# Optimization experiments

Hardware: AMD Instinct MI355X
Metric: run time of the kernel (lower is better)

## Reference

```python
import jax, jax.numpy as jnp
from jax import lax
import numpy as np

NUM_CLASSES = 80
STRIDES = (8, 16, 32)
CONF_THRE = 0.01
NMS_THRE = 0.65
TOPK = 500  # fixed pre-NMS candidate cap (jit-compatible stand-in for dynamic conf filter)


def setup_inputs() -> dict:
    key = jax.random.key(0)
    k8, k16, k32 = jax.random.split(key, 3)
    B, C = 8, 5 + NUM_CLASSES
    return {
        "out8": jax.random.normal(k8, (B, C, 160, 160), dtype=jnp.float32),
        "out16": jax.random.normal(k16, (B, C, 80, 80), dtype=jnp.float32),
        "out32": jax.random.normal(k32, (B, C, 40, 40), dtype=jnp.float32),
    }


def _decode_level(x, stride):
    # x: [B, C, H, W] -> decoded [B, H*W, C]
    B, C, H, W = x.shape
    x = x.reshape(B, C, H * W).transpose(0, 2, 1)  # [B, HW, C]
    yv, xv = jnp.meshgrid(jnp.arange(H), jnp.arange(W), indexing="ij")
    grid = jnp.stack([xv, yv], axis=-1).reshape(1, H * W, 2).astype(x.dtype)
    s = jnp.asarray(stride, x.dtype)
    xy = (x[..., 0:2] + grid) * s
    wh = jnp.exp(x[..., 2:4]) * s
    obj = jax.nn.sigmoid(x[..., 4:5])
    cls = jax.nn.sigmoid(x[..., 5:])
    return jnp.concatenate([xy, wh, obj, cls], axis=-1)


def _iou_one_vs_all(box, boxes):
    # box: [4] xyxy, boxes: [K,4] xyxy
    x1 = jnp.maximum(box[0], boxes[:, 0])
    y1 = jnp.maximum(box[1], boxes[:, 1])
    x2 = jnp.minimum(box[2], boxes[:, 2])
    y2 = jnp.minimum(box[3], boxes[:, 3])
    inter = jnp.maximum(x2 - x1, 0.0) * jnp.maximum(y2 - y1, 0.0)
    a1 = jnp.maximum(box[2] - box[0], 0.0) * jnp.maximum(box[3] - box[1], 0.0)
    a2 = jnp.maximum(boxes[:, 2] - boxes[:, 0], 0.0) * jnp.maximum(boxes[:, 3] - boxes[:, 1], 0.0)
    return inter / (a1 + a2 - inter + 1e-9)


def _nms_keep(boxes, valid, iou_thr):
    # boxes are pre-sorted by descending score; returns bool keep mask [K]
    K = boxes.shape[0]
    idx = jnp.arange(K)

    def body(i, state):
        keep, suppressed = state
        cur_ok = jnp.logical_not(suppressed[i])
        keep = keep.at[i].set(cur_ok)
        iou = _iou_one_vs_all(boxes[i], boxes)
        suppressed = suppressed | ((iou > iou_thr) & cur_ok & (idx > i))
        return keep, suppressed

    keep, _ = lax.fori_loop(0, K, body, (jnp.zeros(K, bool), jnp.logical_not(valid)))
    return keep


def _post_process_image(pred):
    # pred: [N, 5+num_classes] decoded, boxes already xyxy
    cls_scores = pred[:, 5:5 + NUM_CLASSES]
    class_conf = jnp.max(cls_scores, axis=1)
    class_pred = jnp.argmax(cls_scores, axis=1)
    obj = pred[:, 4]
    total = obj * class_conf  # NMS score, same as torchvision call
    masked = jnp.where(total >= CONF_THRE, total, -1.0)
    top_sc, top_i = lax.top_k(masked, TOPK)  # sorted descending
    boxes = pred[top_i, :4]
    obj_k = obj[top_i]
    cc_k = class_conf[top_i]
    lab_k = class_pred[top_i]
    valid = top_sc >= CONF_THRE
    # class-aware (batched) NMS via per-class coordinate offset, as torchvision does
    max_c = jnp.max(jnp.where(valid[:, None], boxes, 0.0)) + 1.0
    boxes_off = boxes + (lab_k.astype(boxes.dtype) * max_c)[:, None]
    keep = _nms_keep(boxes_off, valid, NMS_THRE)
    det = jnp.concatenate(
        [boxes, obj_k[:, None], cc_k[:, None], lab_k.astype(boxes.dtype)[:, None]], axis=1
    )  # [K, 7] = (x1,y1,x2,y2,obj,class_conf,class_id)
    return det * keep[:, None].astype(det.dtype)


def reference(out8, out16, out32):
    levels = [(out8, 8), (out16, 16), (out32, 32)]
    pred = jnp.concatenate([_decode_level(x, s) for x, s in levels], axis=1)  # [B, N, C]
    # cxcywh -> xyxy corners
    cx, cy, w, h = pred[..., 0], pred[..., 1], pred[..., 2], pred[..., 3]
    corners = jnp.stack([cx - w / 2, cy - h / 2, cx + w / 2, cy + h / 2], axis=-1)
    pred = jnp.concatenate([corners, pred[..., 4:]], axis=-1)
    return jax.vmap(_post_process_image)(pred)  # [B, TOPK, 7], zero-padded
```

## Files before the change

### kernel.cpp

```cpp
#include <hip/hip_runtime.h>

#define NPI    33600
#define KTOP   500
#define CAP    1024
#define KEY001 0xBC23D70Au
#define NGRP   1024
#define NIMG   8
#define GPW    525

__device__ __forceinline__ float sigmoidf_(float x) {
  return 1.0f / (1.0f + expf(-x));
}
__device__ __forceinline__ unsigned fkey(float f) {
  unsigned u = __float_as_uint(f);
  return (u & 0x80000000u) ? ~u : (u | 0x80000000u);
}

__global__ __launch_bounds__(128) void k_decode(
    const float* __restrict__ p8, const float* __restrict__ p16,
    const float* __restrict__ p32,
    unsigned* __restrict__ keys, float* __restrict__ dets,
    unsigned* __restrict__ hist2)
{
  const int b  = blockIdx.y;
  const int tx = blockIdx.x;
  const float* lvl; int HW, W, S, j0, abase;
  if (tx < 50)      { lvl = p8;  HW = 25600; W = 160; S = 8;  j0 = tx * 512;        abase = 0; }
  else if (tx < 63) { lvl = p16; HW = 6400;  W = 80;  S = 16; j0 = (tx - 50) * 512; abase = 25600; }
  else              { lvl = p32; HW = 1600;  W = 40;  S = 32; j0 = (tx - 63) * 512; abase = 32000; }
  __shared__ unsigned lh[NGRP];
  for (int i = threadIdx.x; i < NGRP; i += 128) lh[i] = 0;
  __syncthreads();

  const int e = j0 + 4 * threadIdx.x;
  const bool act = (e < HW);
  if (act) {
    const float* base = lvl + (size_t)b * 85 * HW + e;
    float4 t0 = *(const float4*)(base);
    float4 t1 = *(const float4*)(base + (size_t)1 * HW);
    float4 t2 = *(const float4*)(base + (size_t)2 * HW);
    float4 t3 = *(const float4*)(base + (size_t)3 * HW);
    float4 t4 = *(const float4*)(base + (size_t)4 * HW);
    float cc[4] = {-1.0f, -1.0f, -1.0f, -1.0f};
    int   lab[4] = {0, 0, 0, 0};
    for (int c0 = 5; c0 < 85; c0 += 16) {
      float4 r[16];
      #pragma unroll
      for (int u = 0; u < 16; ++u)
        r[u] = *(const float4*)(base + (size_t)(c0 + u) * HW);
      #pragma unroll
      for (int u = 0; u < 16; ++u) {
        float s;
        s = sigmoidf_(r[u].x); if (s > cc[0]) { cc[0] = s; lab[0] = c0 + u - 5; }
        s = sigmoidf_(r[u].y); if (s > cc[1]) { cc[1] = s; lab[1] = c0 + u - 5; }
        s = sigmoidf_(r[u].z); if (s > cc[2]) { cc[2] = s; lab[2] = c0 + u - 5; }
        s = sigmoidf_(r[u].w); if (s > cc[3]) { cc[3] = s; lab[3] = c0 + u - 5; }
      }
    }
    float e0[4] = {t0.x, t0.y, t0.z, t0.w};
    float e1[4] = {t1.x, t1.y, t1.z, t1.w};
    float e2[4] = {t2.x, t2.y, t2.z, t2.w};
    float e3[4] = {t3.x, t3.y, t3.z, t3.w};
    float e4[4] = {t4.x, t4.y, t4.z, t4.w};
    unsigned k4[4];
    float dv[7][4];
    #pragma unroll
    for (int q = 0; q < 4; ++q) {
      float obj = sigmoidf_(e4[q]);
      float tot = obj * cc[q];
      k4[q] = fkey(tot >= 0.01f ? tot : -1.0f);
      int jj = e + q;
      int gy = jj / W, gx = jj - gy * W;
      float fs = (float)S;
      float cx = (e0[q] + (float)gx) * fs;
      float cy = (e1[q] + (float)gy) * fs;
      float w  = expf(e2[q]) * fs;
      float h  = expf(e3[q]) * fs;
      dv[0][q] = cx - 0.5f * w; dv[1][q] = cy - 0.5f * h;
      dv[2][q] = cx + 0.5f * w; dv[3][q] = cy + 0.5f * h;
      dv[4][q] = obj; dv[5][q] = cc[q]; dv[6][q] = (float)lab[q];
    }
    const int a = abase + e;
    *(uint4*)(keys + (size_t)b * NPI + a) = make_uint4(k4[0], k4[1], k4[2], k4[3]);
    const size_t P  = (size_t)NIMG * NPI;
    const size_t pa = (size_t)b * NPI + a;
    #pragma unroll
    for (int c = 0; c < 7; ++c)
      *(float4*)(dets + (size_t)c * P + pa) =
          make_float4(dv[c][0], dv[c][1], dv[c][2], dv[c][3]);
    #pragma unroll
    for (int q = 0; q < 4; ++q) atomicAdd(&lh[k4[q] >> 22], 1u);
  }
  __syncthreads();
  unsigned* gb = hist2 + (size_t)b * NGRP;
  for (int i = threadIdx.x; i < NGRP; i += 128) {
    unsigned v = lh[i];
    if (v) atomicAdd(&gb[i], v);
  }
}

__global__ __launch_bounds__(1024) void k_select(
    const unsigned* __restrict__ hist2, const unsigned* __restrict__ keys,
    const float* __restrict__ dets,
    float* __restrict__ topdet, float* __restrict__ soa,
    unsigned* __restrict__ invalg)
{
  const int b    = blockIdx.x;
  const int tid  = threadIdx.x;
  const int lane = tid & 63;
  const int wave = tid >> 6;

  __shared__ unsigned lh[NGRP];
  __shared__ unsigned sh_sub[4096];
  __shared__ unsigned sh_c64[64];
  __shared__ unsigned sh_G, sh_T;
  __shared__ __align__(16) unsigned long long sh_cand[CAP];
  __shared__ float sh_det[KTOP][7];
  __shared__ unsigned sh_inval[16];
  __shared__ unsigned sh_wcA[16], sh_wcB[16];
  __shared__ float sh_red[16];
  __shared__ float sh_maxc;

  lh[tid] = hist2[(size_t)b * NGRP + tid];
  for (int i = tid; i < 4096; i += 1024) sh_sub[i] = 0;
  __syncthreads();
  if (tid < 64) {
    unsigned s = 0;
    #pragma unroll
    for (int k = 0; k < 16; ++k) s += lh[tid * 16 + k];
    sh_c64[tid] = s;
  }
  __syncthreads();
  if (tid == 0) {
    unsigned cum = 0; int C = 0;
    for (int g = 63; g >= 0; --g) {
      unsigned v = sh_c64[g];
      if (cum + v >= KTOP) { C = g; break; }
      cum += v;
    }
    int G = C * 16; unsigned chi = cum;
    for (int g = C * 16 + 15; g >= C * 16; --g) {
      unsigned v = lh[g];
      if (chi + v >= KTOP) { G = g; break; }
      chi += v;
    }
    sh_G = (unsigned)G;
    sh_c64[0] = chi;
  }
  __syncthreads();
  const unsigned G = sh_G;
  const unsigned* kb = keys + (size_t)b * NPI;

  for (int g = tid; g < NPI / 4; g += 1024) {
    uint4 kv = ((const uint4*)kb)[g];
    unsigned kk[4] = {kv.x, kv.y, kv.z, kv.w};
    #pragma unroll
    for (int q = 0; q < 4; ++q)
      if ((kk[q] >> 22) == G) atomicAdd(&sh_sub[(kk[q] >> 10) & 4095u], 1u);
  }
  __syncthreads();
  unsigned chi10 = sh_c64[0];
  __syncthreads();
  if (tid < 64) {
    unsigned s = 0;
    for (int k = 0; k < 64; ++k) s += sh_sub[tid * 64 + k];
    sh_c64[tid] = s;
  }
  __syncthreads();
  if (tid == 0) {
    unsigned c = chi10; int C2 = 0;
    for (int g = 63; g >= 0; --g) {
      unsigned v = sh_c64[g];
      if (c + v >= KTOP) { C2 = g; break; }
      c += v;
    }
    int T12 = C2 * 64;
    for (int t2 = C2 * 64 + 63; t2 >= C2 * 64; --t2) {
      unsigned v = sh_sub[t2];
      if (c + v >= KTOP) { T12 = t2; break; }
      c += v;
    }
    sh_T = (G << 12) | (unsigned)T12;
  }
  __syncthreads();
  const unsigned T = sh_T;

  unsigned runA = 0, runB = 0;
  for (int it = 0; it < 9; ++it) {
    int gl = it * 64 + lane;
    bool act = (gl < GPW);
    int g = wave * GPW + gl;
    uint4 kv = act ? ((const uint4*)kb)[g] : make_uint4(0, 0, 0, 0);
    unsigned kk[4] = {kv.x, kv.y, kv.z, kv.w};
    #pragma unroll
    for (int q = 0; q < 4; ++q) {
      unsigned bin = kk[q] >> 10;
      runA += (unsigned)__popcll(__ballot(act && (bin > T)));
      runB += (unsigned)__popcll(__ballot(act && (bin == T)));
    }
  }
  if (lane == 0) { sh_wcA[wave] = runA; sh_wcB[wave] = runB; }
  __syncthreads();
  unsigned pA = 0, pB = 0, nA = 0, nBtot = 0;
  #pragma unroll
  for (int w2 = 0; w2 < 16; ++w2) {
    unsigned va = sh_wcA[w2], vb = sh_wcB[w2];
    if (w2 < wave) { pA += va; pB += vb; }
    nA += va; nBtot += vb;
  }
  const unsigned Bcap = CAP - nA;
  const unsigned nBk  = (nBtot < Bcap) ? nBtot : Bcap;
  const int nTot = (int)(nA + nBk);

  for (int it = 0; it < 9; ++it) {
    int gl = it * 64 + lane;
    bool act = (gl < GPW);
    int g = wave * GPW + gl;
    uint4 kv = act ? ((const uint4*)kb)[g] : make_uint4(0, 0, 0, 0);
    unsigned kk[4] = {kv.x, kv.y, kv.z, kv.w};
    bool iA[4], iB[4];
    unsigned long long balA[4], balB[4];
    #pragma unroll
    for (int q = 0; q < 4; ++q) {
      unsigned bin = kk[q] >> 10;
      iA[q] = act && (bin > T);
      iB[q] = act && (bin == T);
      balA[q] = __ballot(iA[q]);
      balB[q] = __ballot(iB[q]);
    }
    unsigned long long lt = (1ULL << lane) - 1ULL;
    unsigned pAl = pA, pBl = pB;
    #pragma unroll
    for (int q = 0; q < 4; ++q) {
      pAl += (unsigned)__popcll(balA[q] & lt);
      pBl += (unsigned)__popcll(balB[q] & lt);
    }
    #pragma unroll
    for (int q = 0; q < 4; ++q) {
      int a0 = g * 4 + q;
      unsigned long long packed =
          ((unsigned long long)kk[q] << 32) |
          (unsigned long long)(0xFFFFFFFFu - (unsigned)a0);
      if (iA[q]) { sh_cand[pAl] = packed; ++pAl; }
      if (iB[q]) { if (pBl < Bcap) sh_cand[nA + pBl] = packed; ++pBl; }
      pA += (unsigned)__popcll(balA[q]);
      pB += (unsigned)__popcll(balB[q]);
    }
  }
  __syncthreads();
  for (int s = nTot + tid; s < CAP; s += 1024) sh_cand[s] = 0ULL;
  __syncthreads();

  for (unsigned kk2 = 2; kk2 <= CAP; kk2 <<= 1) {
    for (unsigned jj = kk2 >> 1; jj > 0; jj >>= 1) {
      unsigned i = (unsigned)tid, p = i ^ jj;
      if (p > i) {
        unsigned long long x = sh_cand[i], y = sh_cand[p];
        bool desc = ((i & kk2) == 0);
        if ((x < y) == desc) { sh_cand[i] = y; sh_cand[p] = x; }
      }
      __syncthreads();
    }
  }

  bool validk = false;
  float contrib = -INFINITY;
  float det[7] = {0, 0, 0, 0, 0, 0, 0};
  if (tid < KTOP) {
    unsigned long long v = sh_cand[tid];
    unsigned keyk = (unsigned)(v >> 32);
    int a = (int)(0xFFFFFFFFu - (unsigned)(v & 0xFFFFFFFFull));
    if (a < 0) a = 0;
    const size_t P  = (size_t)NIMG * NPI;
    const size_t pa = (size_t)b * NPI + (size_t)a;
    #pragma unroll
    for (int c = 0; c < 7; ++c) det[c] = dets[(size_t)c * P + pa];
    #pragma unroll
    for (int c = 0; c < 7; ++c) sh_det[tid][c] = det[c];
    validk = (keyk >= KEY001);
    float m4 = fmaxf(fmaxf(det[0], det[1]), fmaxf(det[2], det[3]));
    contrib = validk ? m4 : 0.0f;
  }
  float r = contrib;
  #pragma unroll
  for (int off = 32; off > 0; off >>= 1) r = fmaxf(r, __shfl_xor(r, off));
  if (lane == 0) sh_red[wave] = r;
  unsigned long long bv = __ballot((tid < KTOP) && !validk);
  if (wave < 8 && lane == 0) {
    sh_inval[wave * 2]     = (unsigned)(bv & 0xFFFFFFFFull);
    sh_inval[wave * 2 + 1] = (unsigned)(bv >> 32);
  }
  __syncthreads();
  if (tid == 0) {
    float m = -INFINITY;
    for (int w2 = 0; w2 < 16; ++w2) m = fmaxf(m, sh_red[w2]);
    sh_maxc = m + 1.0f;
  }
  __syncthreads();
  const float maxc = sh_maxc;
  if (tid < 512) {
    float x1, y1, x2, y2, ar;
    if (tid < KTOP) {
      float offb = det[6] * maxc;
      x1 = det[0] + offb; y1 = det[1] + offb;
      x2 = det[2] + offb; y2 = det[3] + offb;
      ar = fmaxf(x2 - x1, 0.0f) * fmaxf(y2 - y1, 0.0f);
    } else { x1 = y1 = x2 = y2 = ar = 0.0f; }
    soa[(0 * NIMG + b) * 512 + tid] = x1;
    soa[(1 * NIMG + b) * 512 + tid] = y1;
    soa[(2 * NIMG + b) * 512 + tid] = x2;
    soa[(3 * NIMG + b) * 512 + tid] = y2;
    soa[(4 * NIMG + b) * 512 + tid] = ar;
  }
  if (tid < 16) invalg[b * 16 + tid] = sh_inval[tid];
  for (int x = tid; x < KTOP * 7; x += 1024)
    topdet[(size_t)b * (KTOP * 7) + x] = ((const float*)sh_det)[x];
}

__global__ __launch_bounds__(256) void k_iou(
    const float* __restrict__ soa, unsigned* __restrict__ gmask)
{
  const int w = blockIdx.x, b = blockIdx.y;
  const int tid = threadIdx.x;
  __shared__ float sx1[512], sy1[512], sx2[512], sy2[512], sa[512];
  for (int x = tid; x < 512; x += 256) {
    sx1[x] = soa[(0 * NIMG + b) * 512 + x];
    sy1[x] = soa[(1 * NIMG + b) * 512 + x];
    sx2[x] = soa[(2 * NIMG + b) * 512 + x];
    sy2[x] = soa[(3 * NIMG + b) * 512 + x];
    sa[x]  = soa[(4 * NIMG + b) * 512 + x];
  }
  __syncthreads();
  const int jbase = w * 32;
  for (int i = tid; i < KTOP; i += 256) {
    unsigned bits = 0u;
    if (jbase + 31 > i) {
      float ix1 = sx1[i], iy1 = sy1[i], ix2 = sx2[i], iy2 = sy2[i];
      float a1 = sa[i];
      #pragma unroll 4
      for (int jj = 0; jj < 32; ++jj) {
        int j = jbase + jj;
        if (j < KTOP && j > i) {
          float jx1 = sx1[j], jy1 = sy1[j];
          float jx2 = sx2[j], jy2 = sy2[j];
          float a2  = sa[j];
          float iw = fminf(ix2, jx2) - fmaxf(ix1, jx1);
          float ih = fminf(iy2, jy2) - fmaxf(iy1, jy1);
          float inter = fmaxf(iw, 0.0f) * fmaxf(ih, 0.0f);
          if (inter > 0.65f * (a1 + a2 - inter + 1e-9f)) bits |= (1u << jj);
        }
      }
    }
    gmask[((size_t)b * 16 + w) * 512 + i] = bits;
  }
}

__global__ __launch_bounds__(256) void k_nms(
    const unsigned* __restrict__ gmask, const unsigned* __restrict__ invalg,
    const float* __restrict__ topdet, float* __restrict__ out)
{
  const int b = blockIdx.x;
  const int tid = threadIdx.x;
  const int lane = tid & 63;
  __shared__ unsigned sm[KTOP * 17];
  __shared__ unsigned sh_keep[16];
  for (int g = tid; g < KTOP * 16; g += 256) {
    int w = g / KTOP, i = g - w * KTOP;
    sm[i * 17 + w] = gmask[((size_t)b * 16 + w) * 512 + i];
  }
  __syncthreads();
  if (tid < 64) {
    unsigned sup   = (lane < 16) ? invalg[b * 16 + lane] : 0u;
    unsigned keepw = 0u;
    unsigned cur = (unsigned)__builtin_amdgcn_readlane((int)sup, 0);
    unsigned mA = (lane < 16) ? sm[0 * 17 + lane] : 0u;
    unsigned mB = (lane < 16) ? sm[1 * 17 + lane] : 0u;
    for (int i = 0; i < KTOP; i += 2) {
      bool ok = ((cur >> (i & 31)) & 1u) == 0u;
      if (ok) {
        sup |= mA;
        if (lane == (i >> 5)) keepw |= (1u << (i & 31));
      }
      cur = (unsigned)__builtin_amdgcn_readlane((int)sup, (i + 1) >> 5);
      mA = (lane < 16 && (i + 2) < KTOP) ? sm[(i + 2) * 17 + lane] : 0u;
      bool ok2 = ((cur >> ((i + 1) & 31)) & 1u) == 0u;
      if (ok2) {
        sup |= mB;
        if (lane == ((i + 1) >> 5)) keepw |= (1u << ((i + 1) & 31));
      }
      cur = (unsigned)__builtin_amdgcn_readlane((int)sup, (i + 2) >> 5);
      mB = (lane < 16 && (i + 3) < KTOP) ? sm[(i + 3) * 17 + lane] : 0u;
    }
    if (lane < 16) sh_keep[lane] = keepw;
  }
  __syncthreads();
  for (int x = tid; x < KTOP * 7; x += 256) {
    int k = x / 7;
    float keepf = ((sh_keep[k >> 5] >> (k & 31)) & 1u) ? 1.0f : 0.0f;
    out[(size_t)b * (KTOP * 7) + x] = topdet[(size_t)b * (KTOP * 7) + x] * keepf;
  }
}

extern "C" void kernel_launch(void* const* d_in, const int* in_sizes, int n_in,
                              void* d_out, int out_size, void* d_ws, size_t ws_size,
                              hipStream_t stream) {
  const float* p8  = (const float*)d_in[0];
  const float* p16 = (const float*)d_in[1];
  const float* p32 = (const float*)d_in[2];
  float* out = (float*)d_out;
  unsigned* hist2  = (unsigned*)d_ws;
  unsigned* keys   = hist2 + (size_t)NIMG * NGRP;
  float*    dets   = (float*)(keys + (size_t)NIMG * NPI);
  float*    topdet = dets + (size_t)7 * NIMG * NPI;
  float*    soa    = topdet + (size_t)NIMG * KTOP * 7;
  unsigned* invalg = (unsigned*)(soa + (size_t)5 * NIMG * 512);
  unsigned* gmask  = invalg + NIMG * 16;

  hipMemsetAsync(hist2, 0, (size_t)NIMG * NGRP * 4, stream);
  k_decode<<<dim3(67, NIMG), 128, 0, stream>>>(p8, p16, p32, keys, dets, hist2);
  k_select<<<dim3(NIMG), 1024, 0, stream>>>(hist2, keys, dets, topdet, soa, invalg);
  k_iou<<<dim3(16, NIMG), 256, 0, stream>>>(soa, gmask);
  k_nms<<<dim3(NIMG), 256, 0, stream>>>(gmask, invalg, topdet, out);
}
```

Before: 210.0 us.

## Score anchors with raw max-logit and decode only the selected top-K boxes

```diff
diff --git a/kernel.cpp b/kernel.cpp
--- a/kernel.cpp
+++ b/kernel.cpp
@@ -16,84 +16,45 @@
   return (u & 0x80000000u) ? ~u : (u | 0x80000000u);
 }
 
-__global__ __launch_bounds__(128) void k_decode(
+__global__ __launch_bounds__(256) void k_score(
     const float* __restrict__ p8, const float* __restrict__ p16,
     const float* __restrict__ p32,
-    unsigned* __restrict__ keys, float* __restrict__ dets,
-    unsigned* __restrict__ hist2)
+    unsigned* __restrict__ keys, unsigned* __restrict__ hist2)
 {
   const int b  = blockIdx.y;
   const int tx = blockIdx.x;
-  const float* lvl; int HW, W, S, j0, abase;
-  if (tx < 50)      { lvl = p8;  HW = 25600; W = 160; S = 8;  j0 = tx * 512;        abase = 0; }
-  else if (tx < 63) { lvl = p16; HW = 6400;  W = 80;  S = 16; j0 = (tx - 50) * 512; abase = 25600; }
-  else              { lvl = p32; HW = 1600;  W = 40;  S = 32; j0 = (tx - 63) * 512; abase = 32000; }
+  const float* lvl; int HW, j0, abase;
+  if (tx < 50)      { lvl = p8;  HW = 25600; j0 = tx * 512;        abase = 0; }
+  else if (tx < 63) { lvl = p16; HW = 6400;  j0 = (tx - 50) * 512; abase = 25600; }
+  else              { lvl = p32; HW = 1600;  j0 = (tx - 63) * 512; abase = 32000; }
   __shared__ unsigned lh[NGRP];
-  for (int i = threadIdx.x; i < NGRP; i += 128) lh[i] = 0;
-  __syncthreads();
-
-  const int e = j0 + 4 * threadIdx.x;
-  const bool act = (e < HW);
-  if (act) {
+  for (int i = threadIdx.x; i < NGRP; i += 256) lh[i] = 0;
+  __syncthreads();
+
+  const int e = j0 + 2 * threadIdx.x;
+  if (e < HW) {
     const float* base = lvl + (size_t)b * 85 * HW + e;
-    float4 t0 = *(const float4*)(base);
-    float4 t1 = *(const float4*)(base + (size_t)1 * HW);
-    float4 t2 = *(const float4*)(base + (size_t)2 * HW);
-    float4 t3 = *(const float4*)(base + (size_t)3 * HW);
-    float4 t4 = *(const float4*)(base + (size_t)4 * HW);
-    float cc[4] = {-1.0f, -1.0f, -1.0f, -1.0f};
-    int   lab[4] = {0, 0, 0, 0};
+    float2 o2 = *(const float2*)(base + (size_t)4 * HW);
+    float m0 = -INFINITY, m1 = -INFINITY;
     for (int c0 = 5; c0 < 85; c0 += 16) {
-      float4 r[16];
+      float2 r[16];
       #pragma unroll
       for (int u = 0; u < 16; ++u)
-        r[u] = *(const float4*)(base + (size_t)(c0 + u) * HW);
+        r[u] = *(const float2*)(base + (size_t)(c0 + u) * HW);
       #pragma unroll
-      for (int u = 0; u < 16; ++u) {
-        float s;
-        s = sigmoidf_(r[u].x); if (s > cc[0]) { cc[0] = s; lab[0] = c0 + u - 5; }
-        s = sigmoidf_(r[u].y); if (s > cc[1]) { cc[1] = s; lab[1] = c0 + u - 5; }
-        s = sigmoidf_(r[u].z); if (s > cc[2]) { cc[2] = s; lab[2] = c0 + u - 5; }
-        s = sigmoidf_(r[u].w); if (s > cc[3]) { cc[3] = s; lab[3] = c0 + u - 5; }
-      }
-    }
-    float e0[4] = {t0.x, t0.y, t0.z, t0.w};
-    float e1[4] = {t1.x, t1.y, t1.z, t1.w};
-    float e2[4] = {t2.x, t2.y, t2.z, t2.w};
-    float e3[4] = {t3.x, t3.y, t3.z, t3.w};
-    float e4[4] = {t4.x, t4.y, t4.z, t4.w};
-    unsigned k4[4];
-    float dv[7][4];
-    #pragma unroll
-    for (int q = 0; q < 4; ++q) {
-      float obj = sigmoidf_(e4[q]);
-      float tot = obj * cc[q];
-      k4[q] = fkey(tot >= 0.01f ? tot : -1.0f);
-      int jj = e + q;
-      int gy = jj / W, gx = jj - gy * W;
-      float fs = (float)S;
-      float cx = (e0[q] + (float)gx) * fs;
-      float cy = (e1[q] + (float)gy) * fs;
-      float w  = expf(e2[q]) * fs;
-      float h  = expf(e3[q]) * fs;
-      dv[0][q] = cx - 0.5f * w; dv[1][q] = cy - 0.5f * h;
-      dv[2][q] = cx + 0.5f * w; dv[3][q] = cy + 0.5f * h;
-      dv[4][q] = obj; dv[5][q] = cc[q]; dv[6][q] = (float)lab[q];
-    }
-    const int a = abase + e;
-    *(uint4*)(keys + (size_t)b * NPI + a) = make_uint4(k4[0], k4[1], k4[2], k4[3]);
-    const size_t P  = (size_t)NIMG * NPI;
-    const size_t pa = (size_t)b * NPI + a;
-    #pragma unroll
-    for (int c = 0; c < 7; ++c)
-      *(float4*)(dets + (size_t)c * P + pa) =
-          make_float4(dv[c][0], dv[c][1], dv[c][2], dv[c][3]);
-    #pragma unroll
-    for (int q = 0; q < 4; ++q) atomicAdd(&lh[k4[q] >> 22], 1u);
+      for (int u = 0; u < 16; ++u) { m0 = fmaxf(m0, r[u].x); m1 = fmaxf(m1, r[u].y); }
+    }
+    float s0 = sigmoidf_(o2.x) * sigmoidf_(m0);
+    float s1 = sigmoidf_(o2.y) * sigmoidf_(m1);
+    unsigned k0 = fkey(s0 >= 0.01f ? s0 : -1.0f);
+    unsigned k1 = fkey(s1 >= 0.01f ? s1 : -1.0f);
+    *(uint2*)(keys + (size_t)b * NPI + abase + e) = make_uint2(k0, k1);
+    atomicAdd(&lh[k0 >> 22], 1u);
+    atomicAdd(&lh[k1 >> 22], 1u);
   }
   __syncthreads();
   unsigned* gb = hist2 + (size_t)b * NGRP;
-  for (int i = threadIdx.x; i < NGRP; i += 128) {
+  for (int i = threadIdx.x; i < NGRP; i += 256) {
     unsigned v = lh[i];
     if (v) atomicAdd(&gb[i], v);
   }
@@ -101,9 +62,7 @@
 
 __global__ __launch_bounds__(1024) void k_select(
     const unsigned* __restrict__ hist2, const unsigned* __restrict__ keys,
-    const float* __restrict__ dets,
-    float* __restrict__ topdet, float* __restrict__ soa,
-    unsigned* __restrict__ invalg)
+    unsigned* __restrict__ selanch, unsigned* __restrict__ invalg)
 {
   const int b    = blockIdx.x;
   const int tid  = threadIdx.x;
@@ -115,11 +74,8 @@
   __shared__ unsigned sh_c64[64];
   __shared__ unsigned sh_G, sh_T;
   __shared__ __align__(16) unsigned long long sh_cand[CAP];
-  __shared__ float sh_det[KTOP][7];
   __shared__ unsigned sh_inval[16];
   __shared__ unsigned sh_wcA[16], sh_wcB[16];
-  __shared__ float sh_red[16];
-  __shared__ float sh_maxc;
 
   lh[tid] = hist2[(size_t)b * NGRP + tid];
   for (int i = tid; i < 4096; i += 1024) sh_sub[i] = 0;
@@ -263,72 +219,121 @@
     }
   }
 
-  bool validk = false;
-  float contrib = -INFINITY;
-  float det[7] = {0, 0, 0, 0, 0, 0, 0};
   if (tid < KTOP) {
     unsigned long long v = sh_cand[tid];
     unsigned keyk = (unsigned)(v >> 32);
     int a = (int)(0xFFFFFFFFu - (unsigned)(v & 0xFFFFFFFFull));
     if (a < 0) a = 0;
-    const size_t P  = (size_t)NIMG * NPI;
-    const size_t pa = (size_t)b * NPI + (size_t)a;
-    #pragma unroll
-    for (int c = 0; c < 7; ++c) det[c] = dets[(size_t)c * P + pa];
-    #pragma unroll
-    for (int c = 0; c < 7; ++c) sh_det[tid][c] = det[c];
-    validk = (keyk >= KEY001);
-    float m4 = fmaxf(fmaxf(det[0], det[1]), fmaxf(det[2], det[3]));
-    contrib = validk ? m4 : 0.0f;
-  }
-  float r = contrib;
-  #pragma unroll
-  for (int off = 32; off > 0; off >>= 1) r = fmaxf(r, __shfl_xor(r, off));
-  if (lane == 0) sh_red[wave] = r;
-  unsigned long long bv = __ballot((tid < KTOP) && !validk);
-  if (wave < 8 && lane == 0) {
-    sh_inval[wave * 2]     = (unsigned)(bv & 0xFFFFFFFFull);
-    sh_inval[wave * 2 + 1] = (unsigned)(bv >> 32);
-  }
-  __syncthreads();
-  if (tid == 0) {
-    float m = -INFINITY;
-    for (int w2 = 0; w2 < 16; ++w2) m = fmaxf(m, sh_red[w2]);
-    sh_maxc = m + 1.0f;
-  }
-  __syncthreads();
-  const float maxc = sh_maxc;
-  if (tid < 512) {
-    float x1, y1, x2, y2, ar;
-    if (tid < KTOP) {
-      float offb = det[6] * maxc;
-      x1 = det[0] + offb; y1 = det[1] + offb;
-      x2 = det[2] + offb; y2 = det[3] + offb;
-      ar = fmaxf(x2 - x1, 0.0f) * fmaxf(y2 - y1, 0.0f);
-    } else { x1 = y1 = x2 = y2 = ar = 0.0f; }
-    soa[(0 * NIMG + b) * 512 + tid] = x1;
-    soa[(1 * NIMG + b) * 512 + tid] = y1;
-    soa[(2 * NIMG + b) * 512 + tid] = x2;
-    soa[(3 * NIMG + b) * 512 + tid] = y2;
-    soa[(4 * NIMG + b) * 512 + tid] = ar;
-  }
+    selanch[b * KTOP + tid] = (unsigned)a;
+    bool validk = (keyk >= KEY001);
+    unsigned long long bv = __ballot(!validk);
+    if (lane == 0) {
+      sh_inval[wave * 2]     = (unsigned)(bv & 0xFFFFFFFFull);
+      sh_inval[wave * 2 + 1] = (unsigned)(bv >> 32);
+    }
+  } else {
+    unsigned long long bv = __ballot(false);
+    (void)bv;
+  }
+  __syncthreads();
   if (tid < 16) invalg[b * 16 + tid] = sh_inval[tid];
-  for (int x = tid; x < KTOP * 7; x += 1024)
-    topdet[(size_t)b * (KTOP * 7) + x] = ((const float*)sh_det)[x];
+}
+
+__global__ __launch_bounds__(256) void k_gather(
+    const float* __restrict__ p8, const float* __restrict__ p16,
+    const float* __restrict__ p32,
+    const unsigned* __restrict__ selanch, float* __restrict__ seldet)
+{
+  const int b    = blockIdx.y;
+  const int part = blockIdx.x;
+  const int tid  = threadIdx.x;
+  const int p    = tid & 15;
+  const int grp  = tid >> 4;
+  const int lane = tid & 63;
+  const int g0   = lane & ~15;
+
+  for (int iter = 0; iter < 4; ++iter) {
+    int s = part * 64 + iter * 16 + grp;
+    if (s >= KTOP) continue;
+    int a = (int)selanch[b * KTOP + s];
+    const float* lvl; int j, W, HW, S;
+    if (a < 25600)      { lvl = p8;  j = a;         W = 160; HW = 25600; S = 8;  }
+    else if (a < 32000) { lvl = p16; j = a - 25600; W = 80;  HW = 6400;  S = 16; }
+    else                { lvl = p32; j = a - 32000; W = 40;  HW = 1600;  S = 32; }
+    const float* base = lvl + (size_t)b * 85 * HW + j;
+    float cc = -1.0f; int lab = 0;
+    #pragma unroll
+    for (int u = 0; u < 5; ++u) {
+      int c = p + 16 * u;
+      float sv = sigmoidf_(base[(size_t)(5 + c) * HW]);
+      if (sv > cc) { cc = sv; lab = c; }
+    }
+    float tload = (p < 5) ? base[(size_t)p * HW] : 0.0f;
+    #pragma unroll
+    for (int off = 1; off < 16; off <<= 1) {
+      float occ = __shfl_xor(cc, off);
+      int  olb = __shfl_xor(lab, off);
+      if (occ > cc || (occ == cc && olb < lab)) { cc = occ; lab = olb; }
+    }
+    float t0 = __shfl(tload, g0 + 0);
+    float t1 = __shfl(tload, g0 + 1);
+    float t2 = __shfl(tload, g0 + 2);
+    float t3 = __shfl(tload, g0 + 3);
+    float t4 = __shfl(tload, g0 + 4);
+    if (p == 0) {
+      int gy = j / W, gx = j - gy * W;
+      float fs = (float)S;
+      float cx = (t0 + (float)gx) * fs;
+      float cy = (t1 + (float)gy) * fs;
+      float w  = expf(t2) * fs;
+      float h  = expf(t3) * fs;
+      float obj = sigmoidf_(t4);
+      float* d = seldet + ((size_t)b * KTOP + s) * 7;
+      d[0] = cx - 0.5f * w; d[1] = cy - 0.5f * h;
+      d[2] = cx + 0.5f * w; d[3] = cy + 0.5f * h;
+      d[4] = obj; d[5] = cc; d[6] = (float)lab;
+    }
+  }
 }
 
 __global__ __launch_bounds__(256) void k_iou(
-    const float* __restrict__ soa, unsigned* __restrict__ gmask)
+    const float* __restrict__ seldet, const unsigned* __restrict__ invalg,
+    unsigned* __restrict__ gmask)
 {
   const int w = blockIdx.x, b = blockIdx.y;
   const int tid = threadIdx.x;
+  const int lane = tid & 63;
+  const int wave = tid >> 6;
+  __shared__ float sd[KTOP * 7];
   __shared__ float sx1[512], sy1[512], sx2[512], sy2[512], sa[512];
-  for (int x = tid; x < 512; x += 256) {
-    sx1[x] = soa[(0 * NIMG + b) * 512 + x];
-    sy1[x] = soa[(1 * NIMG + b) * 512 + x];
-    sx2[x] = soa[(2 * NIMG + b) * 512 + x];
-    sy2[x] = soa[(3 * NIMG + b) * 512 + x];
-    sa[x]  = soa[(4 * NIMG + b) * 512 + x];
+  __shared__ float sred[4];
+  __shared__ float smaxc;
+  for (int x = tid; x < KTOP * 7; x += 256)
+    sd[x] = seldet[(size_t)b * (KTOP * 7) + x];
+  __syncthreads();
+  float contrib = 0.0f;
+  for (int i = tid; i < KTOP; i += 256) {
+    bool valid = ((invalg[b * 16 + (i >> 5)] >> (i & 31)) & 1u) == 0u;
+    float m4 = fmaxf(fmaxf(sd[i * 7 + 0], sd[i * 7 + 1]),
+                     fmaxf(sd[i * 7 + 2], sd[i * 7 + 3]));
+    contrib = fmaxf(contrib, valid ? m4 : 0.0f);
+  }
+  #pragma unroll
+  for (int off = 32; off > 0; off >>= 1) contrib = fmaxf(contrib, __shfl_xor(contrib, off));
+  if (lane == 0) sred[wave] = contrib;
+  __syncthreads();
+  if (tid == 0) smaxc = fmaxf(fmaxf(sred[0], sred[1]), fmaxf(sred[2], sred[3])) + 1.0f;
+  __syncthreads();
+  const float maxc = smaxc;
+  for (int i = tid; i < 512; i += 256) {
+    float x1, y1, x2, y2, ar;
+    if (i < KTOP) {
+      float offb = sd[i * 7 + 6] * maxc;
+      x1 = sd[i * 7 + 0] + offb; y1 = sd[i * 7 + 1] + offb;
+      x2 = sd[i * 7 + 2] + offb; y2 = sd[i * 7 + 3] + offb;
+      ar = fmaxf(x2 - x1, 0.0f) * fmaxf(y2 - y1, 0.0f);
+    } else { x1 = y1 = x2 = y2 = ar = 0.0f; }
+    sx1[i] = x1; sy1[i] = y1; sx2[i] = x2; sy2[i] = y2; sa[i] = ar;
   }
   __syncthreads();
   const int jbase = w * 32;
@@ -357,7 +362,7 @@
 
 __global__ __launch_bounds__(256) void k_nms(
     const unsigned* __restrict__ gmask, const unsigned* __restrict__ invalg,
-    const float* __restrict__ topdet, float* __restrict__ out)
+    const float* __restrict__ seldet, float* __restrict__ out)
 {
   const int b = blockIdx.x;
   const int tid = threadIdx.x;
@@ -397,7 +402,7 @@
   for (int x = tid; x < KTOP * 7; x += 256) {
     int k = x / 7;
     float keepf = ((sh_keep[k >> 5] >> (k & 31)) & 1u) ? 1.0f : 0.0f;
-    out[(size_t)b * (KTOP * 7) + x] = topdet[(size_t)b * (KTOP * 7) + x] * keepf;
+    out[(size_t)b * (KTOP * 7) + x] = seldet[(size_t)b * (KTOP * 7) + x] * keepf;
   }
 }
 
@@ -408,17 +413,17 @@
   const float* p16 = (const float*)d_in[1];
   const float* p32 = (const float*)d_in[2];
   float* out = (float*)d_out;
-  unsigned* hist2  = (unsigned*)d_ws;
-  unsigned* keys   = hist2 + (size_t)NIMG * NGRP;
-  float*    dets   = (float*)(keys + (size_t)NIMG * NPI);
-  float*    topdet = dets + (size_t)7 * NIMG * NPI;
-  float*    soa    = topdet + (size_t)NIMG * KTOP * 7;
-  unsigned* invalg = (unsigned*)(soa + (size_t)5 * NIMG * 512);
-  unsigned* gmask  = invalg + NIMG * 16;
+  unsigned* hist2   = (unsigned*)d_ws;
+  unsigned* keys    = hist2 + (size_t)NIMG * NGRP;
+  unsigned* selanch = keys + (size_t)NIMG * NPI;
+  unsigned* invalg  = selanch + (size_t)NIMG * KTOP;
+  unsigned* gmask   = invalg + NIMG * 16;
+  float*    seldet  = (float*)(gmask + (size_t)NIMG * 16 * 512);
 
   hipMemsetAsync(hist2, 0, (size_t)NIMG * NGRP * 4, stream);
-  k_decode<<<dim3(67, NIMG), 128, 0, stream>>>(p8, p16, p32, keys, dets, hist2);
-  k_select<<<dim3(NIMG), 1024, 0, stream>>>(hist2, keys, dets, topdet, soa, invalg);
-  k_iou<<<dim3(16, NIMG), 256, 0, stream>>>(soa, gmask);
-  k_nms<<<dim3(NIMG), 256, 0, stream>>>(gmask, invalg, topdet, out);
-}
+  k_score <<<dim3(67, NIMG), 256, 0, stream>>>(p8, p16, p32, keys, hist2);
+  k_select<<<dim3(NIMG), 1024, 0, stream>>>(hist2, keys, selanch, invalg);
+  k_gather<<<dim3(8, NIMG), 256, 0, stream>>>(p8, p16, p32, selanch, seldet);
+  k_iou   <<<dim3(16, NIMG), 256, 0, stream>>>(seldet, invalg, gmask);
+  k_nms   <<<dim3(NIMG), 256, 0, stream>>>(gmask, invalg, seldet, out);
+}
```

Result: faster. 201.9 us (-3.9%).
